# Kernel tuning notes

Hardware: AMD Instinct MI355X
Metric: run time of the kernel (lower is better)

The kernel has to match this reference:

```python
import jax, jax.numpy as jnp
import numpy as np


def _segsum(x):
    """Stable segment-sum. x: (..., l) -> (..., l, l) lower-triangular sums."""
    l = x.shape[-1]
    cs = jnp.cumsum(x, axis=-1)
    seg = cs[..., :, None] - cs[..., None, :]
    mask = jnp.tril(jnp.ones((l, l), dtype=bool))
    return jnp.where(mask, seg, -jnp.inf)


def setup_inputs() -> dict:
    key = jax.random.key(0)
    kx, ka, kb, kc = jax.random.split(key, 4)
    b, s, h, p, n = 4, 8192, 32, 64, 16
    X = jax.random.normal(kx, (b, s, h, p), dtype=jnp.float32)
    # negative A for realistic decaying SSM dynamics / numerical safety
    A = -jnp.abs(jax.random.normal(ka, (b, s, h), dtype=jnp.float32)) * 0.5
    B = jax.random.normal(kb, (b, s, h, n), dtype=jnp.float32)
    C = jax.random.normal(kc, (b, s, h, n), dtype=jnp.float32)
    return {"X": X, "A": A, "B": B, "C": C, "block_len": 64}


def reference(X, A, B, C, block_len):
    b, s, h, p = X.shape
    n = B.shape[-1]
    c = s // block_len
    l = block_len
    # chunk: (b, c, l, ...)
    Xb = X.reshape(b, c, l, h, p)
    Bb = B.reshape(b, c, l, h, n)
    Cb = C.reshape(b, c, l, h, n)
    Ab = A.reshape(b, c, l, h).transpose(0, 3, 1, 2)  # (b, h, c, l)
    A_cumsum = jnp.cumsum(Ab, axis=-1)                # (b, h, c, l)

    # 1) intra-chunk (diagonal) output
    L = jnp.exp(_segsum(Ab))                          # (b, h, c, l, l)
    Y_diag = jnp.einsum("bclhn,bcshn,bhcls,bcshp->bclhp", Cb, Bb, L, Xb)

    # 2) intra-chunk states (chunk-final state contribution)
    decay_states = jnp.exp(A_cumsum[..., -1:] - A_cumsum)   # (b, h, c, l)
    states = jnp.einsum("bclhn,bhcl,bclhp->bchpn", Bb, decay_states, Xb)

    # 3) inter-chunk recurrence (zero initial states)
    A_last = A_cumsum[..., -1]                        # (b, h, c)
    decay_chunk = jnp.exp(_segsum(jnp.pad(A_last, ((0, 0), (0, 0), (1, 0)))))  # (b,h,c+1,c+1)
    states = jnp.concatenate([jnp.zeros_like(states[:, :1]), states], axis=1)  # (b,c+1,h,p,n)
    new_states = jnp.einsum("bhzc,bchpn->bzhpn", decay_chunk, states)
    states = new_states[:, :-1]                       # states entering each chunk

    # 4) state -> output (off-diagonal)
    state_decay_out = jnp.exp(A_cumsum)               # (b, h, c, l)
    Y_off = jnp.einsum("bclhn,bchpn,bhcl->bclhp", Cb, states, state_decay_out)

    Y = (Y_diag + Y_off).reshape(b, s, h, p)
    return Y
```

## Files before the change

kernel.cpp:

```cpp
#include <hip/hip_runtime.h>

#define BB 4
#define SS 8192
#define HH 32
#define PP 64
#define NN 16
#define LL 64
#define CC 128
#define NCHAIN (BB * HH)
#define NCHT (NCHAIN * CC)
#define ITERS 8
#define GRID1 (NCHT / ITERS)

typedef __attribute__((ext_vector_type(8))) short bf16x8;
typedef __attribute__((ext_vector_type(4))) short s16x4;
typedef __attribute__((ext_vector_type(4))) float f32x4;

__device__ inline short f2bf(float f) {
    unsigned u = __builtin_bit_cast(unsigned, f);
    u = (u + 0x7FFFu + ((u >> 16) & 1u)) >> 16;
    return (short)u;
}
__device__ inline float bf2f(short s) {
    unsigned u = ((unsigned)(unsigned short)s) << 16;
    return __builtin_bit_cast(float, u);
}
__device__ inline float wscan(float v, int l) {
    float x = v;
#pragma unroll
    for (int d = 1; d < 64; d <<= 1) {
        float t = __shfl_up(x, d, 64);
        if (l >= d) x += t;
    }
    return x;
}

__global__ __launch_bounds__(256) void k1_states(
    const float* __restrict__ X, const float* __restrict__ A,
    const float* __restrict__ B, short* __restrict__ states,
    float* __restrict__ alast_g, short* __restrict__ xtf, int do_xtf)
{
    int tid = threadIdx.x;
    int w = tid >> 6, l = tid & 63, g = l >> 4, lr = l & 15;
    int r = tid >> 2, q4 = tid & 3;
    int bid = blockIdx.x;

    __shared__ float Bs[2][LL][17];

    float xrA[16], xrB[16];
    float4 br; float av;

#define K1_LOADS(gc_, xr_) { \
    int h_ = (gc_) & 31, c_ = ((gc_) >> 5) & 127, b_ = (gc_) >> 12; \
    size_t row0_ = (size_t)b_ * SS + (size_t)c_ * LL; \
    const float* Xp_ = X + (row0_ * HH + h_) * PP; \
    av = (A + row0_ * HH + h_)[(size_t)l * HH]; \
    br = *(const float4*)(B + (row0_ * HH + h_) * NN + (size_t)r * (HH * NN) + q4 * 4); \
    _Pragma("unroll") for (int kt_ = 0; kt_ < 2; ++kt_) \
    _Pragma("unroll") for (int e_ = 0; e_ < 8; ++e_) \
        xr_[kt_ * 8 + e_] = Xp_[(size_t)(kt_ * 32 + g * 8 + e_) * (HH * PP) + 16 * w + lr]; }

#define K1_STAGE(qd_, gc_) { \
    float x_ = wscan(av, l); \
    float alast_ = __shfl(x_, 63, 64); \
    float wlr_ = __expf(alast_ - __shfl(x_, r, 64)); \
    Bs[qd_][r][q4 * 4 + 0] = br.x * wlr_; \
    Bs[qd_][r][q4 * 4 + 1] = br.y * wlr_; \
    Bs[qd_][r][q4 * 4 + 2] = br.z * wlr_; \
    Bs[qd_][r][q4 * 4 + 3] = br.w * wlr_; \
    if (tid == 0) { \
        int h_ = (gc_) & 31, c_ = ((gc_) >> 5) & 127, b_ = (gc_) >> 12; \
        alast_g[(b_ * HH + h_) * CC + c_] = alast_; } }

#define K1_COMPUTE(qd_, xr_, gc_) { \
    int h_ = (gc_) & 31, c_ = ((gc_) >> 5) & 127, b_ = (gc_) >> 12; \
    size_t cc_ = (size_t)((b_ * HH + h_) * CC + c_); \
    bf16x8 bt0_, bt1_, xf0_, xf1_; \
    _Pragma("unroll") for (int e_ = 0; e_ < 8; ++e_) { \
        bt0_[e_] = f2bf(Bs[qd_][g * 8 + e_][lr]); \
        bt1_[e_] = f2bf(Bs[qd_][32 + g * 8 + e_][lr]); \
        xf0_[e_] = f2bf(xr_[e_]); xf1_[e_] = f2bf(xr_[8 + e_]); } \
    f32x4 st_ = __builtin_amdgcn_mfma_f32_16x16x32_bf16(bt0_, xf0_, (f32x4)0.f, 0, 0, 0); \
    st_ = __builtin_amdgcn_mfma_f32_16x16x32_bf16(bt1_, xf1_, st_, 0, 0, 0); \
    s16x4 sp_ = { f2bf(st_[0]), f2bf(st_[1]), f2bf(st_[2]), f2bf(st_[3]) }; \
    *(s16x4*)(states + (cc_ << 10) + ((16 * w + lr) << 4) + (g << 2)) = sp_; \
    if (do_xtf) { \
        short* xd_ = xtf + (cc_ << 12); \
        ((bf16x8*)xd_)[tid] = xf0_; \
        ((bf16x8*)xd_)[tid + 256] = xf1_; } }

    K1_LOADS(bid, xrA)
    K1_STAGE(0, bid)
    __syncthreads();
#pragma unroll
    for (int t = 0; t < ITERS; ++t) {
        int gc_c = bid + t * GRID1;
        int gc_n = bid + (t + 1) * GRID1;
        if (t + 1 < ITERS) {
            if (t & 1) { K1_LOADS(gc_n, xrA) } else { K1_LOADS(gc_n, xrB) }
        }
        if (t & 1) { K1_COMPUTE(t & 1, xrB, gc_c) } else { K1_COMPUTE(t & 1, xrA, gc_c) }
        if (t + 1 < ITERS) { K1_STAGE((t & 1) ^ 1, gc_n) }
        __syncthreads();
    }
#undef K1_LOADS
#undef K1_STAGE
#undef K1_COMPUTE
}

__global__ __launch_bounds__(256) void k2_scan(
    short* __restrict__ states, const float* __restrict__ alast_g)
{
    int chain = blockIdx.x >> 2;
    int t = ((blockIdx.x & 3) << 8) + threadIdx.x;
    __shared__ float eal[CC];
    if (threadIdx.x < CC)
        eal[threadIdx.x] = __expf(alast_g[chain * CC + threadIdx.x]);
    __syncthreads();

    short* base = states + ((size_t)chain * CC << 10) + t;
    float P = 0.f;
    for (int c0 = 0; c0 < CC; c0 += 8) {
        short s[8];
#pragma unroll
        for (int u = 0; u < 8; ++u) s[u] = base[(size_t)(c0 + u) << 10];
#pragma unroll
        for (int u = 0; u < 8; ++u) {
            float o = P;
            P = eal[c0 + u] * P + bf2f(s[u]);
            base[(size_t)(c0 + u) << 10] = f2bf(o);
        }
    }
}

__global__ __launch_bounds__(256) void k3_big(
    const float* __restrict__ A, const float* __restrict__ Bm,
    const float* __restrict__ Cm, const short* __restrict__ pin,
    const short* __restrict__ xtf, float* __restrict__ Y)
{
    int tid = threadIdx.x;
    int w = tid >> 6, l = tid & 63, g = l >> 4, lr = l & 15;
    int r = tid >> 2, q4 = tid & 3;
    int bid = blockIdx.x;

    __shared__ short XTF[2][8 * 64 * 8];
    __shared__ short BsF[2][4 * 64 * 8];
    __shared__ short PF[2][4 * 64 * 8];
    __shared__ short ScF[8 * 64 * 8];

    ((bf16x8*)ScF)[w * 128 + l] = (bf16x8)0;
    ((bf16x8*)ScF)[w * 128 + 64 + l] = (bf16x8)0;
    if (tid < 128) {
        ((bf16x8*)PF[0])[(tid >> 5) * 64 + 32 + (tid & 31)] = (bf16x8)0;
        ((bf16x8*)PF[1])[(tid >> 5) * 64 + 32 + (tid & 31)] = (bf16x8)0;
    }
    {
        int zt = tid >> 6, zu = (tid >> 1) & 31, zv = tid & 1;
        ((s16x4*)BsF[0])[(zt * 64 + 32 + zu) * 2 + zv] = (s16x4)0;
        ((s16x4*)BsF[1])[(zt * 64 + 32 + zu) * 2 + zv] = (s16x4)0;
    }

    bf16x8 xv0, xv1, caw_c, caw_n;
    float4 br, cr0 = {0,0,0,0}, cr1 = {0,0,0,0};
    s16x4 pinb; float av;
    float x_c, x_n;

#define K3_LOADS(gc_) { \
    int h_ = (gc_) & 31, c_ = ((gc_) >> 5) & 127, b_ = (gc_) >> 12; \
    size_t row0_ = (size_t)b_ * SS + (size_t)c_ * LL; \
    size_t cc_ = (size_t)((b_ * HH + h_) * CC + c_); \
    const short* xs_ = xtf + (cc_ << 12); \
    xv0 = ((const bf16x8*)xs_)[tid]; \
    xv1 = ((const bf16x8*)xs_)[tid + 256]; \
    av = (A + row0_ * HH + h_)[(size_t)l * HH]; \
    br = *(const float4*)(Bm + (row0_ * HH + h_) * NN + (size_t)r * (HH * NN) + q4 * 4); \
    if (g < 2) { \
        const float* cp_ = Cm + (row0_ * HH + h_) * NN + (size_t)(16 * w + lr) * (HH * NN) + g * 8; \
        cr0 = *(const float4*)cp_; cr1 = *(const float4*)(cp_ + 4); } \
    pinb = *(const s16x4*)(pin + (cc_ << 10) + ((16 * w + lr) << 4) + (g << 2)); }

#define K3_STAGE(qd_) { \
    x_n = wscan(av, l); \
    ((bf16x8*)XTF[qd_])[tid] = xv0; \
    ((bf16x8*)XTF[qd_])[tid + 256] = xv1; \
    int fl_ = (r & 15) + 16 * (q4 >> 1); \
    int jt_ = r >> 4; \
    s16x4 bb_ = { f2bf(br.x), f2bf(br.y), f2bf(br.z), f2bf(br.w) }; \
    ((s16x4*)BsF[qd_])[(jt_ * 64 + fl_) * 2 + (q4 & 1)] = bb_; \
    ((s16x4*)PF[qd_])[(w * 64 + (g >> 1) * 16 + lr) * 2 + (g & 1)] = pinb; \
    caw_n = (bf16x8)0; \
    if (g < 2) { \
        caw_n[0] = f2bf(cr0.x); caw_n[1] = f2bf(cr0.y); caw_n[2] = f2bf(cr0.z); caw_n[3] = f2bf(cr0.w); \
        caw_n[4] = f2bf(cr1.x); caw_n[5] = f2bf(cr1.y); caw_n[6] = f2bf(cr1.z); caw_n[7] = f2bf(cr1.w); } }

#define K3_COMPUTE(qd_, gc_) { \
    int h_ = (gc_) & 31, c_ = ((gc_) >> 5) & 127, b_ = (gc_) >> 12; \
    size_t row0_ = (size_t)b_ * SS + (size_t)c_ * LL; \
    float* Yp_ = Y + (row0_ * HH + h_) * PP; \
    float cs_i_[4], ei_[4]; \
    int ib_ = 16 * w + 4 * g; \
    _Pragma("unroll") for (int rr_ = 0; rr_ < 4; ++rr_) { \
        cs_i_[rr_] = __shfl(x_c, ib_ + rr_, 64); ei_[rr_] = __expf(cs_i_[rr_]); } \
    f32x4 acc_[4]; \
    _Pragma("unroll") for (int pt_ = 0; pt_ < 4; ++pt_) { \
        bf16x8 pfv_ = ((bf16x8*)PF[qd_])[pt_ * 64 + l]; \
        acc_[pt_] = __builtin_amdgcn_mfma_f32_16x16x32_bf16(caw_c, pfv_, (f32x4)0.f, 0, 0, 0); } \
    _Pragma("unroll") for (int pt_ = 0; pt_ < 4; ++pt_) \
    _Pragma("unroll") for (int rr_ = 0; rr_ < 4; ++rr_) acc_[pt_][rr_] *= ei_[rr_]; \
    for (int jt_ = 0; jt_ <= w; ++jt_) { \
        bf16x8 bw_ = ((bf16x8*)BsF[qd_])[jt_ * 64 + l]; \
        f32x4 sr_ = __builtin_amdgcn_mfma_f32_16x16x32_bf16(caw_c, bw_, (f32x4)0.f, 0, 0, 0); \
        int j_ = jt_ * 16 + lr; \
        float csj_ = __shfl(x_c, j_, 64); \
        int kt2_ = j_ >> 5; \
        int flb_ = 16 * ((j_ >> 3) & 3); \
        _Pragma("unroll") for (int rr_ = 0; rr_ < 4; ++rr_) { \
            int i15_ = g * 4 + rr_; \
            int i_ = 16 * w + i15_; \
            float v_ = (j_ <= i_) ? sr_[rr_] * __expf(cs_i_[rr_] - csj_) : 0.f; \
            ScF[((w * 2 + kt2_) * 64 + i15_ + flb_) * 8 + (j_ & 7)] = f2bf(v_); } } \
    int kts_ = (w >= 2) ? 2 : 1; \
    for (int kt_ = 0; kt_ < kts_; ++kt_) { \
        bf16x8 af_ = ((bf16x8*)ScF)[(w * 2 + kt_) * 64 + l]; \
        _Pragma("unroll") for (int pt_ = 0; pt_ < 4; ++pt_) { \
            bf16x8 xf_ = ((bf16x8*)XTF[qd_])[(kt_ * 4 + pt_) * 64 + l]; \
            acc_[pt_] = __builtin_amdgcn_mfma_f32_16x16x32_bf16(af_, xf_, acc_[pt_], 0, 0, 0); } } \
    _Pragma("unroll") for (int pt_ = 0; pt_ < 4; ++pt_) \
    _Pragma("unroll") for (int rr_ = 0; rr_ < 4; ++rr_) \
        Yp_[(size_t)(16 * w + 4 * g + rr_) * (HH * PP) + pt_ * 16 + lr] = acc_[pt_][rr_]; }

    K3_LOADS(bid)
    K3_STAGE(0)
    x_c = x_n; caw_c = caw_n;
    __syncthreads();
#pragma unroll
    for (int t = 0; t < ITERS; ++t) {
        if (t + 1 < ITERS) { K3_LOADS(bid + (t + 1) * GRID1) }
        K3_COMPUTE(t & 1, bid + t * GRID1)
        if (t + 1 < ITERS) {
            K3_STAGE((t + 1) & 1)
            x_c = x_n; caw_c = caw_n;
        }
        __syncthreads();
    }
#undef K3_LOADS
#undef K3_STAGE
#undef K3_COMPUTE
}

__global__ __launch_bounds__(256) void k3_small(
    const float* __restrict__ X, const float* __restrict__ A,
    const float* __restrict__ Bm, const float* __restrict__ Cm,
    const short* __restrict__ pin, float* __restrict__ Y)
{
    int blk = blockIdx.x;
    int h = blk & (HH - 1);
    int c = (blk >> 5) & (CC - 1);
    int b = blk >> 12;
    int tid = threadIdx.x;
    int w = tid >> 6, l = tid & 63, g = l >> 4, lr = l & 15;
    int chain = b * HH + h;
    int r = tid >> 2, q = tid & 3;

    __shared__ short XTF[8 * 64 * 8];
    __shared__ short ScF[8 * 64 * 8];
    __shared__ short BsF[4 * 64 * 8];
    __shared__ short PF[4 * 64 * 8];

    size_t row0 = (size_t)b * SS + (size_t)c * LL;
    const float* Xp = X + (row0 * HH + h) * PP;
    const float* Bp = Bm + (row0 * HH + h) * NN;
    const float* Cp = Cm + (row0 * HH + h) * NN;
    const float* Ap = A + row0 * HH + h;
    float* Yp = Y + (row0 * HH + h) * PP;

    float av = Ap[(size_t)l * HH];
    float4 br = *(const float4*)(Bp + (size_t)r * (HH * NN) + q * 4);
    float4 cr0 = {0,0,0,0}, cr1 = {0,0,0,0};
    if (g < 2) {
        const float* crp = Cp + (size_t)(16 * w + lr) * (HH * NN) + g * 8;
        cr0 = *(const float4*)crp;
        cr1 = *(const float4*)(crp + 4);
    }
    s16x4 pinb = *(const s16x4*)(pin + (((size_t)(chain * CC + c)) << 10) + ((16 * w + lr) << 4) + (g << 2));
    float xr[16];
#pragma unroll
    for (int si = 0; si < 2; ++si)
#pragma unroll
        for (int e = 0; e < 8; ++e)
            xr[si * 8 + e] = Xp[(size_t)(si * 32 + g * 8 + e) * (HH * PP) + 16 * w + lr];

    float x = wscan(av, l);

    ((bf16x8*)ScF)[w * 128 + l] = (bf16x8)0;
    ((bf16x8*)ScF)[w * 128 + 64 + l] = (bf16x8)0;
    if (tid < 128)
        ((bf16x8*)PF)[(tid >> 5) * 64 + 32 + (tid & 31)] = (bf16x8)0;
    {
        int zt = tid >> 6, zu = (tid >> 1) & 31, zv = tid & 1;
        ((s16x4*)BsF)[(zt * 64 + 32 + zu) * 2 + zv] = (s16x4)0;
    }
    {
        int fl = (r & 15) + 16 * (q >> 1);
        int jt = r >> 4;
        s16x4 bb = { f2bf(br.x), f2bf(br.y), f2bf(br.z), f2bf(br.w) };
        ((s16x4*)BsF)[(jt * 64 + fl) * 2 + (q & 1)] = bb;
    }
    *(s16x4*)&PF[(w * 64 + (g >> 1) * 16 + lr) * 8 + (g & 1) * 4] = pinb;
    bf16x8 caw = (bf16x8)0;
    if (g < 2) {
        caw[0] = f2bf(cr0.x); caw[1] = f2bf(cr0.y);
        caw[2] = f2bf(cr0.z); caw[3] = f2bf(cr0.w);
        caw[4] = f2bf(cr1.x); caw[5] = f2bf(cr1.y);
        caw[6] = f2bf(cr1.z); caw[7] = f2bf(cr1.w);
    }
    __syncthreads();

    float cs_i[4], ei[4];
    int ib = 16 * w + 4 * g;
#pragma unroll
    for (int rr = 0; rr < 4; ++rr) {
        cs_i[rr] = __shfl(x, ib + rr, 64);
        ei[rr] = __expf(cs_i[rr]);
    }

    f32x4 acc[4];
#pragma unroll
    for (int pt = 0; pt < 4; ++pt) {
        bf16x8 pfv = ((bf16x8*)PF)[pt * 64 + l];
        acc[pt] = __builtin_amdgcn_mfma_f32_16x16x32_bf16(caw, pfv, (f32x4)0.f, 0, 0, 0);
    }
#pragma unroll
    for (int pt = 0; pt < 4; ++pt)
#pragma unroll
        for (int rr = 0; rr < 4; ++rr) acc[pt][rr] *= ei[rr];

    for (int jt = 0; jt <= w; ++jt) {
        bf16x8 bw = ((bf16x8*)BsF)[jt * 64 + l];
        f32x4 sr = __builtin_amdgcn_mfma_f32_16x16x32_bf16(caw, bw, (f32x4)0.f, 0, 0, 0);
        int j = jt * 16 + lr;
        float csj = __shfl(x, j, 64);
        int kt2 = j >> 5;
        int flb = 16 * ((j >> 3) & 3);
#pragma unroll
        for (int rr = 0; rr < 4; ++rr) {
            int i15 = g * 4 + rr;
            int i = 16 * w + i15;
            float v = (j <= i) ? sr[rr] * __expf(cs_i[rr] - csj) : 0.f;
            ScF[((w * 2 + kt2) * 64 + i15 + flb) * 8 + (j & 7)] = f2bf(v);
        }
    }

#pragma unroll
    for (int si = 0; si < 2; ++si) {
        bf16x8 xb;
#pragma unroll
        for (int e = 0; e < 8; ++e) xb[e] = f2bf(xr[si * 8 + e]);
        ((bf16x8*)XTF)[tid + si * 256] = xb;
    }
    __syncthreads();

    int kts = (w >= 2) ? 2 : 1;
    for (int kt = 0; kt < kts; ++kt) {
        bf16x8 af = ((bf16x8*)ScF)[(w * 2 + kt) * 64 + l];
#pragma unroll
        for (int pt = 0; pt < 4; ++pt) {
            bf16x8 xf = ((bf16x8*)XTF)[(kt * 4 + pt) * 64 + l];
            acc[pt] = __builtin_amdgcn_mfma_f32_16x16x32_bf16(af, xf, acc[pt], 0, 0, 0);
        }
    }

#pragma unroll
    for (int pt = 0; pt < 4; ++pt)
#pragma unroll
        for (int rr = 0; rr < 4; ++rr)
            Yp[(size_t)(16 * w + 4 * g + rr) * (HH * PP) + pt * 16 + lr] = acc[pt][rr];
}

extern "C" void kernel_launch(void* const* d_in, const int* in_sizes, int n_in,
                              void* d_out, int out_size, void* d_ws, size_t ws_size,
                              hipStream_t stream)
{
    const float* X = (const float*)d_in[0];
    const float* A = (const float*)d_in[1];
    const float* B = (const float*)d_in[2];
    const float* C = (const float*)d_in[3];
    float* Y = (float*)d_out;

    const size_t states_bytes = (size_t)NCHT * 1024 * 2;
    const size_t alast_bytes  = (size_t)NCHT * 4;
    const size_t xtf_bytes    = (size_t)NCHT * 4096 * 2;
    short* states = (short*)d_ws;
    float* alast  = (float*)((char*)d_ws + states_bytes);
    short* xtf    = (short*)((char*)d_ws + states_bytes + alast_bytes);
    int big = (ws_size >= states_bytes + alast_bytes + xtf_bytes) ? 1 : 0;

    dim3 blk(256);
    k1_states<<<dim3(GRID1), blk, 0, stream>>>(X, A, B, states, alast, xtf, big);
    k2_scan<<<dim3(NCHAIN * 4), blk, 0, stream>>>(states, alast);
    if (big)
        k3_big<<<dim3(GRID1), blk, 0, stream>>>(A, B, C, states, xtf, Y);
    else
        k3_small<<<dim3(NCHT), blk, 0, stream>>>(X, A, B, C, states, Y);
}
```

Before: 262.1 us.

## Repartition k3_big work by output p-columns and keep X fragments in registers

Each wave now computes one 16-column slice of P across all 64 rows instead of one 16-row slice, so the X operand fragments stay in registers and are no longer staged through shared memory. The triangular score tiles are spread evenly over the waves with a fixed assignment, and C is staged in shared memory so any wave can read any row tile. exp(cs_i) and exp(-cs_j) are factored to replace per-element exponentials, and the loop is only partially unrolled. In exchange there is an extra barrier between score writing and score consumption, and splitting the exponential could lose precision or overflow.

```diff
diff --git a/kernel.cpp b/kernel.cpp
--- a/kernel.cpp
+++ b/kernel.cpp
@@ -143,24 +143,21 @@
     int r = tid >> 2, q4 = tid & 3;
     int bid = blockIdx.x;
 
-    __shared__ short XTF[2][8 * 64 * 8];
+    __shared__ short ScF[8 * 64 * 8];
     __shared__ short BsF[2][4 * 64 * 8];
-    __shared__ short PF[2][4 * 64 * 8];
-    __shared__ short ScF[8 * 64 * 8];
-
-    ((bf16x8*)ScF)[w * 128 + l] = (bf16x8)0;
-    ((bf16x8*)ScF)[w * 128 + 64 + l] = (bf16x8)0;
+    __shared__ short CsF[2][4 * 64 * 8];
+    __shared__ short PF [2][4 * 64 * 8];
+
+    ((bf16x8*)ScF)[tid] = (bf16x8)0;
+    ((bf16x8*)ScF)[tid + 256] = (bf16x8)0;
     if (tid < 128) {
-        ((bf16x8*)PF[0])[(tid >> 5) * 64 + 32 + (tid & 31)] = (bf16x8)0;
-        ((bf16x8*)PF[1])[(tid >> 5) * 64 + 32 + (tid & 31)] = (bf16x8)0;
-    }
-    {
-        int zt = tid >> 6, zu = (tid >> 1) & 31, zv = tid & 1;
-        ((s16x4*)BsF[0])[(zt * 64 + 32 + zu) * 2 + zv] = (s16x4)0;
-        ((s16x4*)BsF[1])[(zt * 64 + 32 + zu) * 2 + zv] = (s16x4)0;
-    }
-
-    bf16x8 xv0, xv1, caw_c, caw_n;
+        int zs = (tid >> 5) * 64 + 32 + (tid & 31);
+        ((bf16x8*)BsF[0])[zs] = (bf16x8)0;  ((bf16x8*)BsF[1])[zs] = (bf16x8)0;
+        ((bf16x8*)CsF[0])[zs] = (bf16x8)0;  ((bf16x8*)CsF[1])[zs] = (bf16x8)0;
+        ((bf16x8*)PF [0])[zs] = (bf16x8)0;  ((bf16x8*)PF [1])[zs] = (bf16x8)0;
+    }
+
+    bf16x8 xv0n, xv1n, xv0c, xv1c;
     float4 br, cr0 = {0,0,0,0}, cr1 = {0,0,0,0};
     s16x4 pinb; float av;
     float x_c, x_n;
@@ -170,8 +167,8 @@
     size_t row0_ = (size_t)b_ * SS + (size_t)c_ * LL; \
     size_t cc_ = (size_t)((b_ * HH + h_) * CC + c_); \
     const short* xs_ = xtf + (cc_ << 12); \
-    xv0 = ((const bf16x8*)xs_)[tid]; \
-    xv1 = ((const bf16x8*)xs_)[tid + 256]; \
+    xv0n = ((const bf16x8*)xs_)[tid]; \
+    xv1n = ((const bf16x8*)xs_)[tid + 256]; \
     av = (A + row0_ * HH + h_)[(size_t)l * HH]; \
     br = *(const float4*)(Bm + (row0_ * HH + h_) * NN + (size_t)r * (HH * NN) + q4 * 4); \
     if (g < 2) { \
@@ -181,71 +178,95 @@
 
 #define K3_STAGE(qd_) { \
     x_n = wscan(av, l); \
-    ((bf16x8*)XTF[qd_])[tid] = xv0; \
-    ((bf16x8*)XTF[qd_])[tid + 256] = xv1; \
     int fl_ = (r & 15) + 16 * (q4 >> 1); \
     int jt_ = r >> 4; \
     s16x4 bb_ = { f2bf(br.x), f2bf(br.y), f2bf(br.z), f2bf(br.w) }; \
     ((s16x4*)BsF[qd_])[(jt_ * 64 + fl_) * 2 + (q4 & 1)] = bb_; \
     ((s16x4*)PF[qd_])[(w * 64 + (g >> 1) * 16 + lr) * 2 + (g & 1)] = pinb; \
-    caw_n = (bf16x8)0; \
     if (g < 2) { \
-        caw_n[0] = f2bf(cr0.x); caw_n[1] = f2bf(cr0.y); caw_n[2] = f2bf(cr0.z); caw_n[3] = f2bf(cr0.w); \
-        caw_n[4] = f2bf(cr1.x); caw_n[5] = f2bf(cr1.y); caw_n[6] = f2bf(cr1.z); caw_n[7] = f2bf(cr1.w); } }
-
-#define K3_COMPUTE(qd_, gc_) { \
-    int h_ = (gc_) & 31, c_ = ((gc_) >> 5) & 127, b_ = (gc_) >> 12; \
-    size_t row0_ = (size_t)b_ * SS + (size_t)c_ * LL; \
-    float* Yp_ = Y + (row0_ * HH + h_) * PP; \
-    float cs_i_[4], ei_[4]; \
-    int ib_ = 16 * w + 4 * g; \
-    _Pragma("unroll") for (int rr_ = 0; rr_ < 4; ++rr_) { \
-        cs_i_[rr_] = __shfl(x_c, ib_ + rr_, 64); ei_[rr_] = __expf(cs_i_[rr_]); } \
-    f32x4 acc_[4]; \
-    _Pragma("unroll") for (int pt_ = 0; pt_ < 4; ++pt_) { \
-        bf16x8 pfv_ = ((bf16x8*)PF[qd_])[pt_ * 64 + l]; \
-        acc_[pt_] = __builtin_amdgcn_mfma_f32_16x16x32_bf16(caw_c, pfv_, (f32x4)0.f, 0, 0, 0); } \
-    _Pragma("unroll") for (int pt_ = 0; pt_ < 4; ++pt_) \
-    _Pragma("unroll") for (int rr_ = 0; rr_ < 4; ++rr_) acc_[pt_][rr_] *= ei_[rr_]; \
-    for (int jt_ = 0; jt_ <= w; ++jt_) { \
-        bf16x8 bw_ = ((bf16x8*)BsF[qd_])[jt_ * 64 + l]; \
-        f32x4 sr_ = __builtin_amdgcn_mfma_f32_16x16x32_bf16(caw_c, bw_, (f32x4)0.f, 0, 0, 0); \
-        int j_ = jt_ * 16 + lr; \
-        float csj_ = __shfl(x_c, j_, 64); \
-        int kt2_ = j_ >> 5; \
-        int flb_ = 16 * ((j_ >> 3) & 3); \
-        _Pragma("unroll") for (int rr_ = 0; rr_ < 4; ++rr_) { \
-            int i15_ = g * 4 + rr_; \
-            int i_ = 16 * w + i15_; \
-            float v_ = (j_ <= i_) ? sr_[rr_] * __expf(cs_i_[rr_] - csj_) : 0.f; \
-            ScF[((w * 2 + kt2_) * 64 + i15_ + flb_) * 8 + (j_ & 7)] = f2bf(v_); } } \
-    int kts_ = (w >= 2) ? 2 : 1; \
-    for (int kt_ = 0; kt_ < kts_; ++kt_) { \
-        bf16x8 af_ = ((bf16x8*)ScF)[(w * 2 + kt_) * 64 + l]; \
-        _Pragma("unroll") for (int pt_ = 0; pt_ < 4; ++pt_) { \
-            bf16x8 xf_ = ((bf16x8*)XTF[qd_])[(kt_ * 4 + pt_) * 64 + l]; \
-            acc_[pt_] = __builtin_amdgcn_mfma_f32_16x16x32_bf16(af_, xf_, acc_[pt_], 0, 0, 0); } } \
-    _Pragma("unroll") for (int pt_ = 0; pt_ < 4; ++pt_) \
-    _Pragma("unroll") for (int rr_ = 0; rr_ < 4; ++rr_) \
-        Yp_[(size_t)(16 * w + 4 * g + rr_) * (HH * PP) + pt_ * 16 + lr] = acc_[pt_][rr_]; }
+        bf16x8 cw_; \
+        cw_[0]=f2bf(cr0.x); cw_[1]=f2bf(cr0.y); cw_[2]=f2bf(cr0.z); cw_[3]=f2bf(cr0.w); \
+        cw_[4]=f2bf(cr1.x); cw_[5]=f2bf(cr1.y); cw_[6]=f2bf(cr1.z); cw_[7]=f2bf(cr1.w); \
+        ((bf16x8*)CsF[qd_])[w * 64 + g * 16 + lr] = cw_; } }
+
+#define SCORE_TILE(IT, JT, MASK) { \
+    bf16x8 ca_ = ((bf16x8*)CsF[qb])[(IT) * 64 + l]; \
+    bf16x8 bw_ = ((bf16x8*)BsF[qb])[(JT) * 64 + l]; \
+    f32x4 sr_ = __builtin_amdgcn_mfma_f32_16x16x32_bf16(ca_, bw_, (f32x4)0.f, 0, 0, 0); \
+    float csj_ = __shfl(x_c, (JT) * 16 + lr, 64); \
+    float enj_ = __expf(-csj_); \
+    _Pragma("unroll") for (int rr = 0; rr < 4; ++rr) { \
+        float v_ = sr_[rr] * (eii[IT][rr] * enj_); \
+        if (MASK) v_ = ((JT) * 16 + lr <= (IT) * 16 + 4 * g + rr) ? v_ : 0.f; \
+        ScF[(((IT) * 2 + ((JT) >> 1)) * 64 + ((2 * (JT) + (lr >> 3)) & 3) * 16 + 4 * g + rr) * 8 + (lr & 7)] = f2bf(v_); } }
 
     K3_LOADS(bid)
     K3_STAGE(0)
-    x_c = x_n; caw_c = caw_n;
+    x_c = x_n; xv0c = xv0n; xv1c = xv1n;
     __syncthreads();
-#pragma unroll
+
+#pragma unroll 2
     for (int t = 0; t < ITERS; ++t) {
+        int gc = bid + t * GRID1;
+        int qb = t & 1;
         if (t + 1 < ITERS) { K3_LOADS(bid + (t + 1) * GRID1) }
-        K3_COMPUTE(t & 1, bid + t * GRID1)
-        if (t + 1 < ITERS) {
-            K3_STAGE((t + 1) & 1)
-            x_c = x_n; caw_c = caw_n;
-        }
+
+        float eii[4][4];
+#pragma unroll
+        for (int it = 0; it < 4; ++it)
+#pragma unroll
+            for (int rr = 0; rr < 4; ++rr)
+                eii[it][rr] = __expf(__shfl(x_c, 16 * it + 4 * g + rr, 64));
+
+        f32x4 acc[4];
+        {
+            bf16x8 pfw = ((bf16x8*)PF[qb])[w * 64 + l];
+#pragma unroll
+            for (int it = 0; it < 4; ++it) {
+                bf16x8 ca = ((bf16x8*)CsF[qb])[it * 64 + l];
+                acc[it] = __builtin_amdgcn_mfma_f32_16x16x32_bf16(ca, pfw, (f32x4)0.f, 0, 0, 0);
+            }
+#pragma unroll
+            for (int it = 0; it < 4; ++it)
+#pragma unroll
+                for (int rr = 0; rr < 4; ++rr) acc[it][rr] *= eii[it][rr];
+        }
+
+        if (w == 0)      { SCORE_TILE(0,0,true)  SCORE_TILE(2,1,false) SCORE_TILE(3,2,false) }
+        else if (w == 1) { SCORE_TILE(1,0,false) SCORE_TILE(2,2,true)  SCORE_TILE(3,3,true)  }
+        else if (w == 2) { SCORE_TILE(1,1,true)  SCORE_TILE(3,0,false) }
+        else             { SCORE_TILE(2,0,false) SCORE_TILE(3,1,false) }
+
         __syncthreads();
+
+#pragma unroll
+        for (int it = 0; it < 4; ++it) {
+            bf16x8 af0 = ((bf16x8*)ScF)[(it * 2 + 0) * 64 + l];
+            acc[it] = __builtin_amdgcn_mfma_f32_16x16x32_bf16(af0, xv0c, acc[it], 0, 0, 0);
+        }
+#pragma unroll
+        for (int it = 2; it < 4; ++it) {
+            bf16x8 af1 = ((bf16x8*)ScF)[(it * 2 + 1) * 64 + l];
+            acc[it] = __builtin_amdgcn_mfma_f32_16x16x32_bf16(af1, xv1c, acc[it], 0, 0, 0);
+        }
+        {
+            int h_ = gc & 31, c_ = (gc >> 5) & 127, b_ = gc >> 12;
+            size_t row0_ = (size_t)b_ * SS + (size_t)c_ * LL;
+            float* Yp = Y + (row0_ * HH + h_) * PP;
+#pragma unroll
+            for (int it = 0; it < 4; ++it)
+#pragma unroll
+                for (int rr = 0; rr < 4; ++rr)
+                    Yp[(size_t)(16 * it + 4 * g + rr) * (HH * PP) + 16 * w + lr] = acc[it][rr];
+        }
+
+        if (t + 1 < ITERS) { K3_STAGE((t + 1) & 1) }
+        __syncthreads();
+        x_c = x_n; xv0c = xv0n; xv1c = xv1n;
     }
 #undef K3_LOADS
 #undef K3_STAGE
-#undef K3_COMPUTE
+#undef SCORE_TILE
 }
 
 __global__ __launch_bounds__(256) void k3_small(
```

After: 255.4 us. -2.5%, faster.
